# Performance work log

Hardware: AMD Instinct MI355X
Metric: run time of the kernel (lower is better)

The kernel has to match this reference:

```python
import jax, jax.numpy as jnp
import numpy as np
import math

H = 256; W = 256
NUM_CURVES = 256
NUM_SAMPLES = 32
NUM_BEZIERS = 2
BDEG = 5            # Bernstein degree used by the module (bezier_degree+1)
CTRL_STRIDE = 5     # bezier_degree+1; segments share endpoints, wrap (closed curve)
N_CTRL = NUM_BEZIERS * CTRL_STRIDE   # 10 control points per closed curve
PIX_CHUNK = 512
CHOLESKY_BOUND = jnp.array([0.5, 0.0, 0.5], jnp.float32)


def _bernstein():
    # t in linspace(0.007, 0.993, S) exactly as _update_bernstein_cache
    t = jnp.linspace(0.007, 0.993, NUM_SAMPLES)
    i = jnp.arange(BDEG + 1, dtype=jnp.float32)
    comb = jnp.array([math.comb(BDEG, k) for k in range(BDEG + 1)], jnp.float32)
    return comb * (t[:, None] ** i) * ((1.0 - t[:, None]) ** (BDEG - i))  # [S, BDEG+1]


def _render(control_points, features_dc, cholesky, opacity, depth, background):
    Bmat = _bernstein()
    # closed curve: segment k uses control points (k*5 + j) mod 10, j=0..5
    seg_idx = (jnp.arange(NUM_BEZIERS)[:, None] * CTRL_STRIDE
               + jnp.arange(BDEG + 1)[None, :]) % N_CTRL          # [K, 6]
    seg_ctrl = control_points[:, seg_idx]                          # [N, K, 6, 2]
    pts = jnp.einsum('sj,nkjd->nksd', Bmat, seg_ctrl)              # [N, K, S, 2]
    pts = pts.reshape(NUM_CURVES, -1, 2)                           # [N, Gper, 2]
    gper = pts.shape[1]

    # normalized [-1,1] -> pixel coords
    means = (jnp.tanh(pts) * 0.5 + 0.5) * jnp.array([W, H], jnp.float32)
    means = means.reshape(-1, 2)                                   # [G, 2]

    # 2x2 covariance from lower-triangular Cholesky (per curve)
    c = cholesky + CHOLESKY_BOUND[None, :]                         # l11, l21, l22
    s00 = c[:, 0] ** 2
    s01 = c[:, 0] * c[:, 1]
    s11 = c[:, 1] ** 2 + c[:, 2] ** 2
    det = s00 * s11 - s01 ** 2
    conic = jnp.stack([s11 / det, -s01 / det, s00 / det], -1)      # [N, 3]

    rep = lambda a: jnp.repeat(a, gper, axis=0)
    conic_g = rep(conic)                                           # [G, 3]
    color_g = rep(jax.nn.sigmoid(features_dc))                     # [G, 3]
    alpha_g = rep(jax.nn.sigmoid(opacity))[:, 0]                   # [G]
    depth_g = rep(depth)[:, 0]                                     # [G]

    order = jnp.argsort(depth_g)                                   # front-to-back
    means_s = means[order]
    conic_s = conic_g[order]
    color_s = color_g[order]
    alpha_s = alpha_g[order]

    ys, xs = jnp.meshgrid(jnp.arange(H, dtype=jnp.float32) + 0.5,
                          jnp.arange(W, dtype=jnp.float32) + 0.5, indexing='ij')
    pix = jnp.stack([xs.ravel(), ys.ravel()], -1).reshape(-1, PIX_CHUNK, 2)

    @jax.checkpoint
    def render_chunk(p):                                           # [C,2] -> [C,3]
        dx = p[:, None, 0] - means_s[None, :, 0]
        dy = p[:, None, 1] - means_s[None, :, 1]
        power = (-0.5 * (conic_s[None, :, 0] * dx * dx
                         + conic_s[None, :, 2] * dy * dy)
                 - conic_s[None, :, 1] * dx * dy)
        a = jnp.clip(alpha_s[None, :] * jnp.exp(power), 0.0, 0.999)
        logT = jnp.cumsum(jnp.log1p(-a), axis=1)
        t_excl = jnp.exp(logT - jnp.log1p(-a))   # transmittance before each splat
        rgb = (a * t_excl) @ color_s             # [C, 3]
        return rgb + jnp.exp(logT[:, -1:]) * background[None, :]

    img = jax.lax.map(render_chunk, pix)                           # [P/C, C, 3]
    return jnp.clip(img.reshape(H, W, 3), 0.0, 1.0)


def setup_inputs() -> dict:
    key = jax.random.key(0)
    k1, k2, k3, k4 = jax.random.split(key, 4)
    return {
        "control_points": jax.random.normal(k1, (NUM_CURVES, N_CTRL, 2), jnp.float32),
        "features_dc": jax.random.uniform(k2, (NUM_CURVES, 3), jnp.float32),
        "cholesky": jax.random.uniform(k3, (NUM_CURVES, 3), jnp.float32),
        "opacity": jnp.ones((NUM_CURVES, 1), jnp.float32),
        "depth": jax.random.uniform(k4, (NUM_CURVES, 1), jnp.float32),
        "background": jnp.ones((3,), jnp.float32),
    }


def reference(control_points, features_dc, cholesky, opacity, depth, background):
    return _render(control_points, features_dc, cholesky, opacity, depth, background)
```

## Files before the change

kernel.cpp:

```cpp
#include <hip/hip_runtime.h>
#include <math.h>

#define NCURVES   256
#define GPER      64
#define NUM_G     (NCURVES*GPER)
#define IMG_W     256
#define IMG_H     256
#define TILE      16
#define TILES_X   (IMG_W/TILE)
#define TILES_Y   (IMG_H/TILE)
#define NTILES    (TILES_X*TILES_Y)
#define REC_F     12
#define SEGS      4
#define GSEG      (NUM_G/SEGS)

#define A_MIN     3.0e-6f
#define P_CUT     (-12.6f)
#define T_EPS     1.0e-5f

__global__ __launch_bounds__(GPER)
void prep(const float* __restrict__ ctrl,
          const float* __restrict__ features,
          const float* __restrict__ cholesky,
          const float* __restrict__ opacity,
          const float* __restrict__ depth,
          float*       __restrict__ recs,
          unsigned*    __restrict__ bbox)
{
    int c   = blockIdx.x;
    int tid = threadIdx.x;

    float dc = depth[c];
    int r = 0;
    #pragma unroll
    for (int jj = 0; jj < 4; ++jj) {
        int j = tid + jj*64;
        float dj = depth[j];
        r += (dj < dc) || (dj == dc && j < c);
    }
    #pragma unroll
    for (int off = 32; off > 0; off >>= 1) r += __shfl_down(r, off, 64);
    r = __shfl(r, 0, 64);

    float c0 = cholesky[3*c+0] + 0.5f;
    float c1 = cholesky[3*c+1];
    float c2 = cholesky[3*c+2] + 0.5f;
    float s00 = c0*c0;
    float s01 = c0*c1;
    float s11 = c1*c1 + c2*c2;
    float inv = 1.0f / (s00*s11 - s01*s01);
    float A  =  s11*inv;
    float Bc = -s01*inv;
    float Cc =  s00*inv;

    float cr = 1.0f/(1.0f + __expf(-features[3*c+0]));
    float cg = 1.0f/(1.0f + __expf(-features[3*c+1]));
    float cb = 1.0f/(1.0f + __expf(-features[3*c+2]));
    float al = 1.0f/(1.0f + __expf(-opacity[c]));

    float cut = fmaxf(2.0f*(__logf(al) - __logf(A_MIN)), 0.0f);
    float rx = sqrtf(cut * s00);
    float ry = sqrtf(cut * s11);

    int k = tid >> 5;
    int s = tid & 31;
    float t = 0.007f + (float)s * (0.986f/31.0f);
    float u = 1.0f - t;
    float t2=t*t, t3=t2*t, t4=t3*t, t5=t4*t;
    float u2=u*u, u3=u2*u, u4=u3*u, u5=u4*u;
    float w[6] = { u5, 5.0f*t*u4, 10.0f*t2*u3, 10.0f*t3*u2, 5.0f*t4*u, t5 };

    const float* cp = ctrl + c*20;
    float px = 0.0f, py = 0.0f;
    #pragma unroll
    for (int j = 0; j < 6; ++j) {
        int idx = (k*5 + j) % 10;
        px += w[j]*cp[2*idx+0];
        py += w[j]*cp[2*idx+1];
    }
    float mx = (tanhf(px)*0.5f + 0.5f) * (float)IMG_W;
    float my = (tanhf(py)*0.5f + 0.5f) * (float)IMG_H;

    int gi = r*GPER + tid;
    float* o = recs + (size_t)gi*REC_F;
    o[0]=mx; o[1]=my; o[2]=A; o[3]=Bc; o[4]=Cc; o[5]=al;
    o[6]=cr; o[7]=cg; o[8]=cb; o[9]=0.0f; o[10]=0.0f; o[11]=0.0f;

    int tx0 = min(max((int)floorf((mx - rx) * (1.0f/TILE)), 0), TILES_X-1);
    int tx1 = min(max((int)floorf((mx + rx) * (1.0f/TILE)), 0), TILES_X-1);
    int ty0 = min(max((int)floorf((my - ry) * (1.0f/TILE)), 0), TILES_Y-1);
    int ty1 = min(max((int)floorf((my + ry) * (1.0f/TILE)), 0), TILES_Y-1);
    bbox[gi] = (unsigned)tx0 | ((unsigned)ty0<<8) | ((unsigned)tx1<<16) | ((unsigned)ty1<<24);
}

__global__ __launch_bounds__(256)
void render_seg(const float*    __restrict__ recs,
                const unsigned* __restrict__ bbox,
                float4*         __restrict__ partial)
{
    __shared__ float4   data[256][3];
    __shared__ unsigned wcnt[4];

    int tid   = threadIdx.x;
    int seg   = blockIdx.x >> 8;
    int tile  = blockIdx.x & 255;
    int tilex = tile & (TILES_X-1);
    int tiley = tile >> 4;
    int X = tilex*TILE + (tid & (TILE-1));
    int Y = tiley*TILE + (tid >> 4);
    float px = (float)X + 0.5f;
    float py = (float)Y + 0.5f;

    int lane = tid & 63;
    int wid  = tid >> 6;
    unsigned long long lmask = (1ull << lane) - 1ull;

    float T = 1.0f, accr = 0.0f, accg = 0.0f, accb = 0.0f;

    int gbeg = seg * GSEG;
    int gend = gbeg + GSEG;
    for (int base = gbeg; base < gend; base += 256) {
        int g = base + tid;
        unsigned bb = bbox[g];
        int tx0 =  bb        & 0xff;
        int ty0 = (bb >> 8)  & 0xff;
        int tx1 = (bb >> 16) & 0xff;
        int ty1 = (bb >> 24) & 0xff;
        bool pred = (tilex >= tx0) & (tilex <= tx1) & (tiley >= ty0) & (tiley <= ty1);

        unsigned long long m = __ballot(pred ? 1 : 0);
        if (lane == 0) wcnt[wid] = (unsigned)__popcll(m);

        int nalive = __syncthreads_count(T > T_EPS);
        if (nalive == 0) break;

        unsigned c0 = wcnt[0], c1 = wcnt[1], c2 = wcnt[2], c3 = wcnt[3];
        int total = (int)(c0 + c1 + c2 + c3);
        if (pred) {
            unsigned woff = (wid > 0 ? c0 : 0u) + (wid > 1 ? c1 : 0u) + (wid > 2 ? c2 : 0u);
            int slot = (int)(woff + (unsigned)__popcll(m & lmask));
            const float4* rp = (const float4*)(recs + (size_t)g*REC_F);
            float4 d0 = rp[0], d1 = rp[1], d2 = rp[2];
            data[slot][0] = d0;
            data[slot][1] = d1;
            data[slot][2] = d2;
        }
        __syncthreads();

        if (T > T_EPS) {
            for (int j = 0; j < total; ++j) {
                float4 q0 = data[j][0];
                float4 q1 = data[j][1];
                float  cb_ = data[j][2].x;
                float dx = px - q0.x;
                float dy = py - q0.y;
                float p  = -0.5f*(q0.z*dx*dx + q1.x*dy*dy) - q0.w*dx*dy;
                if (p > P_CUT) {
                    float a = q1.y * __expf(p);
                    a = fminf(a, 0.999f);
                    float wgt = a * T;
                    accr += wgt * q1.z;
                    accg += wgt * q1.w;
                    accb += wgt * cb_;
                    T *= (1.0f - a);
                    if (T < T_EPS) break;
                }
            }
        }
    }

    partial[(size_t)seg*(IMG_W*IMG_H) + (size_t)Y*IMG_W + X] =
        make_float4(accr, accg, accb, T);
}

__global__ __launch_bounds__(256)
void combine(const float4* __restrict__ partial,
             const float*  __restrict__ background,
             float*        __restrict__ out)
{
    int p = blockIdx.x * 256 + threadIdx.x;

    float accr = 0.0f, accg = 0.0f, accb = 0.0f, T = 1.0f;
    #pragma unroll
    for (int s = 0; s < SEGS; ++s) {
        float4 q = partial[(size_t)s*(IMG_W*IMG_H) + p];
        accr += T * q.x;
        accg += T * q.y;
        accb += T * q.z;
        T    *= q.w;
    }
    float r = fminf(fmaxf(accr + T*background[0], 0.0f), 1.0f);
    float g = fminf(fmaxf(accg + T*background[1], 0.0f), 1.0f);
    float b = fminf(fmaxf(accb + T*background[2], 0.0f), 1.0f);

    size_t oi = (size_t)p*3;
    out[oi+0] = r;
    out[oi+1] = g;
    out[oi+2] = b;
}

extern "C" void kernel_launch(void* const* d_in, const int* in_sizes, int n_in,
                              void* d_out, int out_size, void* d_ws, size_t ws_size,
                              hipStream_t stream)
{
    const float* ctrl       = (const float*)d_in[0];
    const float* features   = (const float*)d_in[1];
    const float* cholesky   = (const float*)d_in[2];
    const float* opacity    = (const float*)d_in[3];
    const float* depth      = (const float*)d_in[4];
    const float* background = (const float*)d_in[5];
    float* out = (float*)d_out;

    char* w = (char*)d_ws;
    float*    recs    = (float*)   (w);
    unsigned* bboxp   = (unsigned*)(w + 786432);
    float4*   partial = (float4*)  (w + 786432 + 65536);

    prep<<<NCURVES, GPER, 0, stream>>>(ctrl, features, cholesky, opacity, depth,
                                       recs, bboxp);
    render_seg<<<SEGS*NTILES, 256, 0, stream>>>(recs, bboxp, partial);
    combine<<<(IMG_W*IMG_H)/256, 256, 0, stream>>>(partial, background, out);
}
```

Before: 101.4 us.

## Split splats into 16 depth segments and prefetch bbox masks per block

Raises the number of depth segments from 4 to 16, so each tile is rendered by 16 blocks, each handling 1024 splats. This gives 4096 blocks instead of 1024, and the segment index is moved to the low bits of the block id so blocks for the same tile run close together. Each block loads all its bbox words up front, and batches with no overlapping splats skip the shared-memory fill, its barrier and the blend loop. The cost is four times more partial-buffer traffic, a longer combine pass, and less early termination inside each segment.

After: 93.42 us. 7.9% less time.

```diff
diff --git a/kernel.cpp b/kernel.cpp
--- a/kernel.cpp
+++ b/kernel.cpp
@@ -11,8 +11,9 @@
 #define TILES_Y   (IMG_H/TILE)
 #define NTILES    (TILES_X*TILES_Y)
 #define REC_F     12
-#define SEGS      4
+#define SEGS      16
 #define GSEG      (NUM_G/SEGS)
+#define NSUB      (GSEG/256)
 
 #define A_MIN     3.0e-6f
 #define P_CUT     (-12.6f)
@@ -102,8 +103,8 @@
     __shared__ unsigned wcnt[4];
 
     int tid   = threadIdx.x;
-    int seg   = blockIdx.x >> 8;
-    int tile  = blockIdx.x & 255;
+    int seg   = blockIdx.x & (SEGS-1);
+    int tile  = blockIdx.x >> 4;
     int tilex = tile & (TILES_X-1);
     int tiley = tile >> 4;
     int X = tilex*TILE + (tid & (TILE-1));
@@ -115,20 +116,29 @@
     int wid  = tid >> 6;
     unsigned long long lmask = (1ull << lane) - 1ull;
 
+    int gbeg = seg * GSEG;
+
+    bool pred[NSUB];
+    {
+        unsigned bb[NSUB];
+        #pragma unroll
+        for (int b = 0; b < NSUB; ++b) bb[b] = bbox[gbeg + b*256 + tid];
+        #pragma unroll
+        for (int b = 0; b < NSUB; ++b) {
+            unsigned v = bb[b];
+            int tx0 =  v        & 0xff;
+            int ty0 = (v >> 8)  & 0xff;
+            int tx1 = (v >> 16) & 0xff;
+            int ty1 = (v >> 24) & 0xff;
+            pred[b] = (tilex >= tx0) & (tilex <= tx1) & (tiley >= ty0) & (tiley <= ty1);
+        }
+    }
+
     float T = 1.0f, accr = 0.0f, accg = 0.0f, accb = 0.0f;
 
-    int gbeg = seg * GSEG;
-    int gend = gbeg + GSEG;
-    for (int base = gbeg; base < gend; base += 256) {
-        int g = base + tid;
-        unsigned bb = bbox[g];
-        int tx0 =  bb        & 0xff;
-        int ty0 = (bb >> 8)  & 0xff;
-        int tx1 = (bb >> 16) & 0xff;
-        int ty1 = (bb >> 24) & 0xff;
-        bool pred = (tilex >= tx0) & (tilex <= tx1) & (tiley >= ty0) & (tiley <= ty1);
-
-        unsigned long long m = __ballot(pred ? 1 : 0);
+    #pragma unroll 1
+    for (int b = 0; b < NSUB; ++b) {
+        unsigned long long m = __ballot(pred[b] ? 1 : 0);
         if (lane == 0) wcnt[wid] = (unsigned)__popcll(m);
 
         int nalive = __syncthreads_count(T > T_EPS);
@@ -136,34 +146,36 @@
 
         unsigned c0 = wcnt[0], c1 = wcnt[1], c2 = wcnt[2], c3 = wcnt[3];
         int total = (int)(c0 + c1 + c2 + c3);
-        if (pred) {
-            unsigned woff = (wid > 0 ? c0 : 0u) + (wid > 1 ? c1 : 0u) + (wid > 2 ? c2 : 0u);
-            int slot = (int)(woff + (unsigned)__popcll(m & lmask));
-            const float4* rp = (const float4*)(recs + (size_t)g*REC_F);
-            float4 d0 = rp[0], d1 = rp[1], d2 = rp[2];
-            data[slot][0] = d0;
-            data[slot][1] = d1;
-            data[slot][2] = d2;
-        }
-        __syncthreads();
-
-        if (T > T_EPS) {
-            for (int j = 0; j < total; ++j) {
-                float4 q0 = data[j][0];
-                float4 q1 = data[j][1];
-                float  cb_ = data[j][2].x;
-                float dx = px - q0.x;
-                float dy = py - q0.y;
-                float p  = -0.5f*(q0.z*dx*dx + q1.x*dy*dy) - q0.w*dx*dy;
-                if (p > P_CUT) {
-                    float a = q1.y * __expf(p);
-                    a = fminf(a, 0.999f);
-                    float wgt = a * T;
-                    accr += wgt * q1.z;
-                    accg += wgt * q1.w;
-                    accb += wgt * cb_;
-                    T *= (1.0f - a);
-                    if (T < T_EPS) break;
+        if (total) {
+            if (pred[b]) {
+                unsigned woff = (wid > 0 ? c0 : 0u) + (wid > 1 ? c1 : 0u) + (wid > 2 ? c2 : 0u);
+                int slot = (int)(woff + (unsigned)__popcll(m & lmask));
+                const float4* rp = (const float4*)(recs + (size_t)(gbeg + b*256 + tid)*REC_F);
+                float4 d0 = rp[0], d1 = rp[1], d2 = rp[2];
+                data[slot][0] = d0;
+                data[slot][1] = d1;
+                data[slot][2] = d2;
+            }
+            __syncthreads();
+
+            if (T > T_EPS) {
+                for (int j = 0; j < total; ++j) {
+                    float4 q0 = data[j][0];
+                    float4 q1 = data[j][1];
+                    float  cb_ = data[j][2].x;
+                    float dx = px - q0.x;
+                    float dy = py - q0.y;
+                    float p  = -0.5f*(q0.z*dx*dx + q1.x*dy*dy) - q0.w*dx*dy;
+                    if (p > P_CUT) {
+                        float a = q1.y * __expf(p);
+                        a = fminf(a, 0.999f);
+                        float wgt = a * T;
+                        accr += wgt * q1.z;
+                        accg += wgt * q1.w;
+                        accb += wgt * cb_;
+                        T *= (1.0f - a);
+                        if (T < T_EPS) break;
+                    }
                 }
             }
         }
```
